# Kernel tuning notes

Hardware: AMD Instinct MI355X
Metric: run time of the kernel (lower is better)

The kernel has to match this reference:

```python
import jax, jax.numpy as jnp
import numpy as np

EMBED_DIM = 256
NUM_HEADS = 8
WIN = 16


def setup_inputs() -> dict:
    key = jax.random.key(0)
    ks = jax.random.split(key, 10)
    B, C, H, W = 2, EMBED_DIM, 192, 192
    p = 0.02  # weight init scale
    return {
        "x_q": jax.random.normal(ks[0], (B, C, H, W), jnp.float32),
        "x_kv": jax.random.normal(ks[1], (B, C, H, W), jnp.float32),
        "Wq": jax.random.normal(ks[2], (C, C), jnp.float32) * p,
        "bq": jax.random.normal(ks[3], (C,), jnp.float32) * p,
        "Wk": jax.random.normal(ks[4], (C, C), jnp.float32) * p,
        "bk": jax.random.normal(ks[5], (C,), jnp.float32) * p,
        "Wv": jax.random.normal(ks[6], (C, C), jnp.float32) * p,
        "bv": jax.random.normal(ks[7], (C,), jnp.float32) * p,
        "Wo": jax.random.normal(ks[8], (C, C), jnp.float32) * p,
        "bo": jax.random.normal(ks[9], (C,), jnp.float32) * p,
    }


def _proj(x, Wt, b):
    # 1x1 Conv2d: out[b,d,h,w] = sum_c Wt[d,c] * x[b,c,h,w] + b[d]
    return jnp.einsum('bchw,dc->bdhw', x, Wt) + b[None, :, None, None]


def _windowize(t, B, C, nH, nW, heads, hd):
    t = t.reshape(B, C, nH, WIN, nW, WIN).transpose(0, 2, 4, 1, 3, 5)
    return t.reshape(B * nH * nW, heads, hd, WIN * WIN)


def reference(x_q, x_kv, Wq, bq, Wk, bk, Wv, bv, Wo, bo):
    B, C, H, W = x_q.shape
    heads = NUM_HEADS
    hd = C // heads
    scale = hd ** (-0.5)
    nH, nW = H // WIN, W // WIN

    q = _proj(x_q, Wq, bq)
    k = _proj(x_kv, Wk, bk)
    v = _proj(x_kv, Wv, bv)

    q = _windowize(q, B, C, nH, nW, heads, hd).transpose(0, 1, 3, 2)  # (w,h,S,d)
    k = _windowize(k, B, C, nH, nW, heads, hd)                         # (w,h,d,S)
    v = _windowize(v, B, C, nH, nW, heads, hd).transpose(0, 1, 3, 2)  # (w,h,S,d)

    attn = jax.nn.softmax(jnp.einsum('whsd,whdt->whst', q, k) * scale, axis=-1)
    out = jnp.einsum('whst,whtd->whsd', attn, v)  # (w,heads,S,hd)

    out = out.transpose(0, 1, 3, 2).reshape(B * nH * nW, C, WIN, WIN)
    out = out.reshape(B, nH, nW, C, WIN, WIN).transpose(0, 3, 1, 4, 2, 5)
    out = out.reshape(B, C, H, W)

    return _proj(out, Wo, bo)
```

## Files before the change

### kernel.cpp

```cpp
#include <hip/hip_runtime.h>
#include <stdint.h>

typedef unsigned short b16;
typedef unsigned int   u32;
typedef __attribute__((ext_vector_type(8))) short short8;
typedef __attribute__((ext_vector_type(4))) float f32x4;

#define DEVI static __device__ __forceinline__

constexpr int CCH   = 256;
constexpr int IMG   = 192;
constexpr int PLANE = IMG * IMG;
constexpr int WTOK  = 256;
constexpr int WELEM = WTOK * CCH;
constexpr long XN   = 18874368;

DEVI b16 f2bf(float f) {
  u32 u = __float_as_uint(f);
  u += 0x7fffu + ((u >> 16) & 1u);
  return (b16)(u >> 16);
}

DEVI void gl2lds16(const b16* g, b16* l) {
  __builtin_amdgcn_global_load_lds(
      (const __attribute__((address_space(1))) u32*)g,
      (__attribute__((address_space(3))) u32*)l, 16, 0, 0);
}

DEVI short8 lds8(const b16* p) { return *reinterpret_cast<const short8*>(p); }

__global__ __launch_bounds__(192) void prep_kernel(
    const float* __restrict__ xq, const float* __restrict__ xkv,
    const float* __restrict__ Wq, const float* __restrict__ Wk,
    const float* __restrict__ Wv, const float* __restrict__ Wo,
    b16* __restrict__ xw, b16* __restrict__ Wb)
{
  int bid = blockIdx.x, t = threadIdx.x;
  if (bid < 6144) {
    int grp = bid & 7;
    int rem = bid >> 3;
    int y   = rem % 192;
    int bb  = (rem / 192) & 1;
    int inp = rem / 384;
    int c0  = grp * 32;
    int x   = t;
    const float* src = (inp ? xkv : xq)
        + (long)(bb * CCH + c0) * PLANE + y * IMG + x;
    u32 pk[16];
#pragma unroll
    for (int k = 0; k < 16; k++) {
      float lo = src[(long)(2 * k)     * PLANE];
      float hi = src[(long)(2 * k + 1) * PLANE];
      pk[k] = (u32)f2bf(lo) | ((u32)f2bf(hi) << 16);
    }
    int win = bb * 144 + (y >> 4) * 12 + (x >> 4);
    int sp  = (y & 15) * 16 + (x & 15);
    b16* dst = xw + (long)inp * XN + (long)win * WELEM + sp * CCH + c0;
    uint4* d4 = reinterpret_cast<uint4*>(dst);
#pragma unroll
    for (int k = 0; k < 4; k++) {
      uint4 q;
      q.x = pk[4 * k + 0]; q.y = pk[4 * k + 1];
      q.z = pk[4 * k + 2]; q.w = pk[4 * k + 3];
      d4[k] = q;
    }
  } else {
    int idx = (bid - 6144) * 192 + t;
    if (idx < 32768) {
      int p = idx >> 13;
      int r = (idx & 8191) * 8;
      const float* src = (p == 0 ? Wq : p == 1 ? Wk : p == 2 ? Wv : Wo) + r;
      b16 o[8];
#pragma unroll
      for (int j = 0; j < 8; j++) o[j] = f2bf(src[j]);
      uint4 pk;
      pk.x = o[0] | ((u32)o[1] << 16);
      pk.y = o[2] | ((u32)o[3] << 16);
      pk.z = o[4] | ((u32)o[5] << 16);
      pk.w = o[6] | ((u32)o[7] << 16);
      *reinterpret_cast<uint4*>(Wb + p * 65536 + r) = pk;
    }
  }
}

DEVI void btgemm_core(const b16* __restrict__ Aw, const b16* __restrict__ Bt,
                      b16* as_, b16* bs_, int lane, int wid, f32x4 (&acc)[4][4])
{
  int wm = wid >> 1, wn = wid & 1, quad = lane >> 4, l15 = lane & 15;
  for (int kc = 0; kc < 4; kc++) {
    int c0 = kc * 64;
    __syncthreads();
#pragma unroll
    for (int i = 0; i < 4; i++) {
      int it  = wid * 4 + i;
      int row = it * 8 + (lane >> 3);
      int g   = (lane & 7) ^ (row & 7);
      gl2lds16(Aw + row * CCH + c0 + g * 8, as_ + it * 512);
    }
#pragma unroll
    for (int i = 0; i < 2; i++) {
      int it  = wid * 2 + i;
      int row = it * 8 + (lane >> 3);
      int g   = (lane & 7) ^ (row & 7);
      gl2lds16(Bt + row * CCH + c0 + g * 8, bs_ + it * 512);
    }
    __syncthreads();
#pragma unroll
    for (int kk = 0; kk < 2; kk++) {
      short8 af[4], bfv[4];
#pragma unroll
      for (int mt = 0; mt < 4; mt++) {
        int row = wm * 64 + mt * 16 + l15;
        int g   = (kk * 4 + quad) ^ (row & 7);
        af[mt]  = lds8(as_ + row * 64 + g * 8);
      }
#pragma unroll
      for (int nt = 0; nt < 4; nt++) {
        int row = wn * 64 + nt * 16 + l15;
        int g   = (kk * 4 + quad) ^ (row & 7);
        bfv[nt] = lds8(bs_ + row * 64 + g * 8);
      }
#pragma unroll
      for (int mt = 0; mt < 4; mt++)
#pragma unroll
        for (int nt = 0; nt < 4; nt++)
          acc[mt][nt] = __builtin_amdgcn_mfma_f32_16x16x32_bf16(
              af[mt], bfv[nt], acc[mt][nt], 0, 0, 0);
    }
  }
}

__global__ __launch_bounds__(512) void qkv_kernel(
    const b16* __restrict__ xw, const b16* __restrict__ Wb,
    const float* __restrict__ bq, const float* __restrict__ bk,
    const float* __restrict__ bv,
    b16* __restrict__ QW, b16* __restrict__ KW, b16* __restrict__ VT)
{
  __shared__ b16 as_[256 * 64];
  __shared__ b16 bs_[128 * 64];
  int bid  = blockIdx.x;
  int mode = bid / 576;
  int rem  = bid % 576;
  int win  = rem >> 1;
  int sp0  = (rem & 1) * 128;
  const b16* Aw = Wb + mode * 65536;
  const b16* Bt = xw + (mode ? XN : 0) + (long)win * WELEM + sp0 * CCH;
  const float* bias = mode == 0 ? bq : mode == 1 ? bk : bv;
  int lane = threadIdx.x & 63, wid = threadIdx.x >> 6;
  int wm = wid >> 1, wn = wid & 1, quad = lane >> 4, l15 = lane & 15;

  f32x4 acc[4][4];
  const f32x4 ZV = {0.f, 0.f, 0.f, 0.f};
#pragma unroll
  for (int i = 0; i < 4; i++)
#pragma unroll
    for (int j = 0; j < 4; j++) acc[i][j] = ZV;

  btgemm_core(Aw, Bt, as_, bs_, lane, wid, acc);

  if (mode < 2) {
    float qs = (mode == 0) ? 0.25505392f : 1.0f;
    b16* Out = (mode == 0 ? QW : KW) + (long)win * WELEM;
#pragma unroll
    for (int mt = 0; mt < 4; mt++) {
      int d0 = wm * 64 + mt * 16 + quad * 4;
      f32x4 bb = *reinterpret_cast<const f32x4*>(bias + d0);
#pragma unroll
      for (int nt = 0; nt < 4; nt++) {
        int sp = sp0 + wn * 64 + nt * 16 + l15;
        uint2 pk;
        pk.x = f2bf((acc[mt][nt][0] + bb[0]) * qs) | ((u32)f2bf((acc[mt][nt][1] + bb[1]) * qs) << 16);
        pk.y = f2bf((acc[mt][nt][2] + bb[2]) * qs) | ((u32)f2bf((acc[mt][nt][3] + bb[3]) * qs) << 16);
        *reinterpret_cast<uint2*>(Out + (long)sp * CCH + d0) = pk;
      }
    }
  } else {
    b16* Out = VT + (long)win * WELEM;
#pragma unroll
    for (int mt = 0; mt < 4; mt++) {
      int d0 = wm * 64 + mt * 16 + quad * 4;
      f32x4 bb = *reinterpret_cast<const f32x4*>(bias + d0);
#pragma unroll
      for (int nt = 0; nt < 4; nt++) {
        int sp = sp0 + wn * 64 + nt * 16 + l15;
#pragma unroll
        for (int r = 0; r < 4; r++)
          Out[(long)(d0 + r) * WTOK + sp] = f2bf(acc[mt][nt][r] + bb[r]);
      }
    }
  }
}

__global__ __launch_bounds__(256) void attn_kernel(
    const b16* __restrict__ QW, const b16* __restrict__ KW,
    const b16* __restrict__ VT, b16* __restrict__ AW)
{
  __shared__ b16 ks[256 * 32];
  __shared__ b16 vs[32 * 256];
  __shared__ b16 ps[4 * 64 * 40];
  int bid = blockIdx.x;
  int win = bid >> 3, head = bid & 7;
  int lane = threadIdx.x & 63, wid = threadIdx.x >> 6;
  int quad = lane >> 4, l15 = lane & 15;

  const b16* Kg = KW + (long)win * WELEM + head * 32;
  const b16* Vg = VT + (long)win * WELEM + head * 32 * WTOK;
  const b16* Qg = QW + (long)win * WELEM + head * 32;

#pragma unroll
  for (int i = 0; i < 4; i++) {
    int it  = wid * 4 + i;
    int key = it * 16 + (lane >> 2);
    gl2lds16(Kg + key * CCH + (lane & 3) * 8, ks + it * 512);
  }
#pragma unroll
  for (int i = 0; i < 4; i++) {
    int it   = wid * 4 + i;
    int slot = it * 64 + lane;
    int d    = slot >> 5;
    int gp   = slot & 31;
    int g    = (gp & 24) | ((gp & 7) ^ (d & 7));
    gl2lds16(Vg + d * WTOK + g * 8, vs + it * 512);
  }

  short8 qf[4];
#pragma unroll
  for (int qt = 0; qt < 4; qt++) {
    int q = wid * 64 + qt * 16 + l15;
    qf[qt] = *reinterpret_cast<const short8*>(Qg + (long)q * CCH + quad * 8);
  }

  __syncthreads();

  const f32x4 ZV = {0.f, 0.f, 0.f, 0.f};
  f32x4 oacc[2][4];
#pragma unroll
  for (int mt = 0; mt < 2; mt++)
#pragma unroll
    for (int qt = 0; qt < 4; qt++) oacc[mt][qt] = ZV;
  float psum[4];
#pragma unroll
  for (int qt = 0; qt < 4; qt++) psum[qt] = 0.f;

  b16* psw = ps + wid * (64 * 40);

  for (int kb = 0; kb < 8; kb++) {
    int k0 = kb * 32;
    short8 kf[2];
#pragma unroll
    for (int km = 0; km < 2; km++)
      kf[km] = lds8(ks + (k0 + km * 16 + l15) * 32 + quad * 8);
    f32x4 sc[2][4];
#pragma unroll
    for (int km = 0; km < 2; km++)
#pragma unroll
      for (int qt = 0; qt < 4; qt++)
        sc[km][qt] = __builtin_amdgcn_mfma_f32_16x16x32_bf16(kf[km], qf[qt], ZV, 0, 0, 0);

#pragma unroll
    for (int qt = 0; qt < 4; qt++) {
      int qrow = qt * 16 + l15;
#pragma unroll
      for (int km = 0; km < 2; km++) {
        u32 u0 = __float_as_uint(__builtin_amdgcn_exp2f(sc[km][qt][0])) & 0xffff0000u;
        u32 u1 = __float_as_uint(__builtin_amdgcn_exp2f(sc[km][qt][1])) & 0xffff0000u;
        u32 u2 = __float_as_uint(__builtin_amdgcn_exp2f(sc[km][qt][2])) & 0xffff0000u;
        u32 u3 = __float_as_uint(__builtin_amdgcn_exp2f(sc[km][qt][3])) & 0xffff0000u;
        psum[qt] += (__uint_as_float(u0) + __uint_as_float(u1))
                  + (__uint_as_float(u2) + __uint_as_float(u3));
        uint2 pk;
        pk.x = (u0 >> 16) | u1;
        pk.y = (u2 >> 16) | u3;
        *reinterpret_cast<uint2*>(psw + qrow * 40 + km * 16 + quad * 4) = pk;
      }
    }
    short8 vf[2], pf[4];
#pragma unroll
    for (int mt = 0; mt < 2; mt++) {
      int d  = mt * 16 + l15;
      int gl = kb * 4 + quad;
      int gs = (gl & 24) | ((gl & 7) ^ (d & 7));
      vf[mt] = lds8(vs + d * WTOK + gs * 8);
    }
#pragma unroll
    for (int qt = 0; qt < 4; qt++)
      pf[qt] = lds8(psw + (qt * 16 + l15) * 40 + quad * 8);
#pragma unroll
    for (int mt = 0; mt < 2; mt++)
#pragma unroll
      for (int qt = 0; qt < 4; qt++)
        oacc[mt][qt] = __builtin_amdgcn_mfma_f32_16x16x32_bf16(
            vf[mt], pf[qt], oacc[mt][qt], 0, 0, 0);
  }

  b16* Og = AW + (long)win * WELEM + head * 32;
#pragma unroll
  for (int qt = 0; qt < 4; qt++) {
    float l = psum[qt];
    l += __shfl_xor(l, 16);
    l += __shfl_xor(l, 32);
    float rl = __builtin_amdgcn_rcpf(l);
    int q = wid * 64 + qt * 16 + l15;
#pragma unroll
    for (int mt = 0; mt < 2; mt++) {
      uint2 pk;
      pk.x = f2bf(oacc[mt][qt][0] * rl) | ((u32)f2bf(oacc[mt][qt][1] * rl) << 16);
      pk.y = f2bf(oacc[mt][qt][2] * rl) | ((u32)f2bf(oacc[mt][qt][3] * rl) << 16);
      *reinterpret_cast<uint2*>(Og + (long)q * CCH + mt * 16 + quad * 4) = pk;
    }
  }
}

__global__ __launch_bounds__(512) void oproj_kernel(
    const b16* __restrict__ AW, const b16* __restrict__ Wb,
    const float* __restrict__ bo, float* __restrict__ out)
{
  __shared__ b16 as_[256 * 64];
  __shared__ b16 bs_[128 * 64];
  int bid = blockIdx.x;
  int win = bid >> 1;
  int sp0 = (bid & 1) * 128;
  const b16* Aw = Wb + 3 * 65536;
  const b16* Bt = AW + (long)win * WELEM + sp0 * CCH;
  int lane = threadIdx.x & 63, wid = threadIdx.x >> 6;
  int wm = wid >> 1, wn = wid & 1, quad = lane >> 4, l15 = lane & 15;

  f32x4 acc[4][4];
  const f32x4 ZV = {0.f, 0.f, 0.f, 0.f};
#pragma unroll
  for (int i = 0; i < 4; i++)
#pragma unroll
    for (int j = 0; j < 4; j++) acc[i][j] = ZV;

  btgemm_core(Aw, Bt, as_, bs_, lane, wid, acc);

  int b = win / 144, wh = (win / 12) % 12, ww = win % 12;
#pragma unroll
  for (int mt = 0; mt < 4; mt++) {
    int d0 = wm * 64 + mt * 16 + quad * 4;
    f32x4 bb = *reinterpret_cast<const f32x4*>(bo + d0);
#pragma unroll
    for (int nt = 0; nt < 4; nt++) {
      int sp = sp0 + wn * 64 + nt * 16 + l15;
      int y = sp >> 4, x = sp & 15;
      float* op = out + (long)b * CCH * PLANE + (long)(wh * 16 + y) * IMG + ww * 16 + x;
#pragma unroll
      for (int r = 0; r < 4; r++)
        op[(long)(d0 + r) * PLANE] = acc[mt][nt][r] + bb[r];
    }
  }
}

extern "C" void kernel_launch(void* const* d_in, const int* in_sizes, int n_in,
                              void* d_out, int out_size, void* d_ws, size_t ws_size,
                              hipStream_t stream)
{
  const float* xq  = (const float*)d_in[0];
  const float* xkv = (const float*)d_in[1];
  const float* Wq  = (const float*)d_in[2];
  const float* bq  = (const float*)d_in[3];
  const float* Wk  = (const float*)d_in[4];
  const float* bk  = (const float*)d_in[5];
  const float* Wv  = (const float*)d_in[6];
  const float* bv  = (const float*)d_in[7];
  const float* Wo  = (const float*)d_in[8];
  const float* bo  = (const float*)d_in[9];

  char* ws = (char*)d_ws;
  b16* xw = (b16*)ws;
  b16* QW = (b16*)(ws + 75497472);
  b16* KW = (b16*)(ws + 113246208);
  b16* VT = (b16*)(ws + 150994944);
  b16* Wb = (b16*)(ws + 188743680);
  b16* AW = xw;
  float* out = (float*)d_out;

  prep_kernel<<<dim3(6320), dim3(192), 0, stream>>>(xq, xkv, Wq, Wk, Wv, Wo, xw, Wb);
  qkv_kernel<<<dim3(1728), dim3(512), 0, stream>>>(xw, Wb, bq, bk, bv, QW, KW, VT);
  attn_kernel<<<dim3(2304), dim3(256), 0, stream>>>(QW, KW, VT, AW);
  oproj_kernel<<<dim3(576), dim3(512), 0, stream>>>(AW, Wb, bo, out);
}
```

Measured before the change: 370.3 us.

## Stage input transpose through LDS with double-buffered async global loads

The fp32-to-bf16 channel-transpose prep kernel now copies each 32-channel row slab into a swizzled LDS tile with global_load_lds and double-buffers across 8 tiles per persistent block. Conversion and window-layout stores then read from LDS, so each thread no longer issues 32 strided scalar loads. Weight conversion moves to its own small kernel, which adds one launch. Hand-coded waitcnt values and the XOR swizzle make correctness fragile.

```diff
diff --git a/kernel.cpp b/kernel.cpp
--- a/kernel.cpp
+++ b/kernel.cpp
@@ -21,7 +21,7 @@
   return (b16)(u >> 16);
 }
 
-DEVI void gl2lds16(const b16* g, b16* l) {
+DEVI void gl2lds16(const void* g, void* l) {
   __builtin_amdgcn_global_load_lds(
       (const __attribute__((address_space(1))) u32*)g,
       (__attribute__((address_space(3))) u32*)l, 16, 0, 0);
@@ -29,57 +29,108 @@
 
 DEVI short8 lds8(const b16* p) { return *reinterpret_cast<const short8*>(p); }
 
-__global__ __launch_bounds__(192) void prep_kernel(
-    const float* __restrict__ xq, const float* __restrict__ xkv,
+__global__ __launch_bounds__(256) void wprep_kernel(
     const float* __restrict__ Wq, const float* __restrict__ Wk,
     const float* __restrict__ Wv, const float* __restrict__ Wo,
-    b16* __restrict__ xw, b16* __restrict__ Wb)
-{
-  int bid = blockIdx.x, t = threadIdx.x;
-  if (bid < 6144) {
-    int grp = bid & 7;
-    int rem = bid >> 3;
-    int y   = rem % 192;
-    int bb  = (rem / 192) & 1;
-    int inp = rem / 384;
-    int c0  = grp * 32;
-    int x   = t;
-    const float* src = (inp ? xkv : xq)
-        + (long)(bb * CCH + c0) * PLANE + y * IMG + x;
-    u32 pk[16];
-#pragma unroll
-    for (int k = 0; k < 16; k++) {
-      float lo = src[(long)(2 * k)     * PLANE];
-      float hi = src[(long)(2 * k + 1) * PLANE];
-      pk[k] = (u32)f2bf(lo) | ((u32)f2bf(hi) << 16);
-    }
-    int win = bb * 144 + (y >> 4) * 12 + (x >> 4);
-    int sp  = (y & 15) * 16 + (x & 15);
-    b16* dst = xw + (long)inp * XN + (long)win * WELEM + sp * CCH + c0;
-    uint4* d4 = reinterpret_cast<uint4*>(dst);
-#pragma unroll
-    for (int k = 0; k < 4; k++) {
-      uint4 q;
-      q.x = pk[4 * k + 0]; q.y = pk[4 * k + 1];
-      q.z = pk[4 * k + 2]; q.w = pk[4 * k + 3];
-      d4[k] = q;
-    }
-  } else {
-    int idx = (bid - 6144) * 192 + t;
-    if (idx < 32768) {
-      int p = idx >> 13;
-      int r = (idx & 8191) * 8;
-      const float* src = (p == 0 ? Wq : p == 1 ? Wk : p == 2 ? Wv : Wo) + r;
-      b16 o[8];
-#pragma unroll
-      for (int j = 0; j < 8; j++) o[j] = f2bf(src[j]);
-      uint4 pk;
-      pk.x = o[0] | ((u32)o[1] << 16);
-      pk.y = o[2] | ((u32)o[3] << 16);
-      pk.z = o[4] | ((u32)o[5] << 16);
-      pk.w = o[6] | ((u32)o[7] << 16);
-      *reinterpret_cast<uint4*>(Wb + p * 65536 + r) = pk;
-    }
+    b16* __restrict__ Wb)
+{
+  int idx = blockIdx.x * 256 + threadIdx.x;
+  int p = idx >> 13;
+  int r = (idx & 8191) * 8;
+  const float* src = (p == 0 ? Wq : p == 1 ? Wk : p == 2 ? Wv : Wo) + r;
+  b16 o[8];
+#pragma unroll
+  for (int j = 0; j < 8; j++) o[j] = f2bf(src[j]);
+  uint4 pk;
+  pk.x = o[0] | ((u32)o[1] << 16);
+  pk.y = o[2] | ((u32)o[3] << 16);
+  pk.z = o[4] | ((u32)o[5] << 16);
+  pk.w = o[6] | ((u32)o[7] << 16);
+  *reinterpret_cast<uint4*>(Wb + p * 65536 + r) = pk;
+}
+
+constexpr int PREP_NB = 768;
+constexpr int PREP_NT = 8;
+constexpr int LPITCH  = 208;
+
+__global__ __launch_bounds__(256) void prep_kernel(
+    const float* __restrict__ xq, const float* __restrict__ xkv,
+    b16* __restrict__ xw)
+{
+  __shared__ float ls[2][32 * LPITCH];
+  const int bid = blockIdx.x, t = threadIdx.x;
+  const int lane = t & 63, w = t >> 6;
+
+  const int gA = (lane < 48) ? ((lane & 0x30) | (lane & 15)) : (lane - 48);
+  const int gX = (lane < 48) ? 15 : 0;
+  const bool ld_act = (lane < 52);
+
+  for (int i = 0; i < PREP_NT; i++) {
+    if (i == 0) {
+      int tile = bid;
+      int grp = tile & 7, rem = tile >> 3;
+      int y = rem % 192, bb = (rem / 192) & 1, inp = rem / 384;
+      const float* base = (inp ? xkv : xq)
+          + (long)(bb * CCH + grp * 32) * PLANE + (long)y * IMG;
+      if (ld_act) {
+#pragma unroll
+        for (int j = 0; j < 8; j++) {
+          int c = w * 8 + j;
+          int g = gA ^ (gX & c);
+          gl2lds16(base + (long)c * PLANE + g * 4, &ls[0][c * LPITCH]);
+        }
+      }
+    }
+    if (i + 1 < PREP_NT) {
+      int tile = bid + (i + 1) * PREP_NB;
+      int grp = tile & 7, rem = tile >> 3;
+      int y = rem % 192, bb = (rem / 192) & 1, inp = rem / 384;
+      const float* base = (inp ? xkv : xq)
+          + (long)(bb * CCH + grp * 32) * PLANE + (long)y * IMG;
+      if (ld_act) {
+#pragma unroll
+        for (int j = 0; j < 8; j++) {
+          int c = w * 8 + j;
+          int g = gA ^ (gX & c);
+          gl2lds16(base + (long)c * PLANE + g * 4, &ls[(i + 1) & 1][c * LPITCH]);
+        }
+      }
+    }
+    __builtin_amdgcn_sched_barrier(0);
+    if (i == 0)                __builtin_amdgcn_s_waitcnt(0xF78);
+    else if (i + 1 < PREP_NT)  __builtin_amdgcn_s_waitcnt(0xF7B);
+    else                       __builtin_amdgcn_s_waitcnt(0xF73);
+    __builtin_amdgcn_s_barrier();
+    __builtin_amdgcn_sched_barrier(0);
+
+    {
+      int tile = bid + i * PREP_NB;
+      int grp = tile & 7, rem = tile >> 3;
+      int y = rem % 192, bb = (rem / 192) & 1, inp = rem / 384;
+      const float* lsb = ls[i & 1];
+#pragma unroll
+      for (int m = 0; m < 3; m++) {
+        int idx = t + m * 256;
+        int px = idx >> 2, k = idx & 3;
+        int shi = (px >> 2) & 0x30, g4 = (px >> 2) & 15, po = px & 3;
+        u32 d[4];
+#pragma unroll
+        for (int jj = 0; jj < 4; jj++) {
+          int cl = k * 8 + 2 * jj, ch = cl + 1;
+          float lo = lsb[cl * LPITCH + ((shi | (g4 ^ (cl & 15))) << 2) + po];
+          float hi = lsb[ch * LPITCH + ((shi | (g4 ^ (ch & 15))) << 2) + po];
+          d[jj] = (u32)f2bf(lo) | ((u32)f2bf(hi) << 16);
+        }
+        int win = bb * 144 + (y >> 4) * 12 + (px >> 4);
+        int sp  = (y & 15) * 16 + (px & 15);
+        b16* dst = xw + (long)inp * XN + (long)win * WELEM + sp * CCH + grp * 32 + k * 8;
+        uint4 q;
+        q.x = d[0]; q.y = d[1]; q.z = d[2]; q.w = d[3];
+        *reinterpret_cast<uint4*>(dst) = q;
+      }
+    }
+    __builtin_amdgcn_sched_barrier(0);
+    __builtin_amdgcn_s_barrier();
   }
 }
 
@@ -375,7 +426,8 @@
   b16* AW = xw;
   float* out = (float*)d_out;
 
-  prep_kernel<<<dim3(6320), dim3(192), 0, stream>>>(xq, xkv, Wq, Wk, Wv, Wo, xw, Wb);
+  wprep_kernel<<<dim3(128), dim3(256), 0, stream>>>(Wq, Wk, Wv, Wo, Wb);
+  prep_kernel<<<dim3(PREP_NB), dim3(256), 0, stream>>>(xq, xkv, xw);
   qkv_kernel<<<dim3(1728), dim3(512), 0, stream>>>(xw, Wb, bq, bk, bv, QW, KW, VT);
   attn_kernel<<<dim3(2304), dim3(256), 0, stream>>>(QW, KW, VT, AW);
   oproj_kernel<<<dim3(576), dim3(512), 0, stream>>>(AW, Wb, bo, out);
```

After: 346.1 us. 6.5% less time.
